# Optimization experiments

Hardware: AMD Instinct MI355X
Metric: run time of the kernel (lower is better)

Reference implementation:

```python
import jax, jax.numpy as jnp
import numpy as np
from jax import lax

DN = ('NCH', 'OIH', 'NCH')

def conv1d(x, w, b, pad=0):
    y = lax.conv_general_dilated(x, w, window_strides=(1,), padding=[(pad, pad)], dimension_numbers=DN)
    return y + b[None, :, None]

def conv_transpose1d(x, w_torch, b):
    # torch ConvTranspose1d weight: [C_in, C_out, K]; equivalent to full conv with flipped kernel
    k = w_torch.shape[-1]
    w = jnp.flip(jnp.transpose(w_torch, (1, 0, 2)), axis=-1)  # [C_out, C_in, K]
    y = lax.conv_general_dilated(x, w, window_strides=(1,), padding=[(k - 1, k - 1)], dimension_numbers=DN)
    return y + b[None, :, None]

def converter(signal, w1, b1, w2, b2, wt, bt, w3, b3):
    h = jax.nn.relu(conv1d(signal, w1, b1))          # [B,10,n-2]
    h = jax.nn.relu(conv1d(h, w2, b2))               # [B,10,n-2]
    h = jax.nn.relu(conv_transpose1d(h, wt, bt))     # [B,10,n]
    h = jax.nn.sigmoid(conv1d(h, w3, b3))            # [B,2,n]
    return h

def setup_inputs() -> dict:
    key = jax.random.key(0)
    ks = jax.random.split(key, 12)
    B, C, n = 32, 128, 8192
    signal = jax.random.normal(ks[0], (B, C, n), dtype=jnp.float32)
    curr_diag = jax.random.uniform(ks[1], (B, n - 1), dtype=jnp.float32) + 0.5
    s = 0.1
    return {
        'signal': signal,
        'curr_diag': curr_diag,
        'index_diag': 1,
        'w1': jax.random.normal(ks[2], (10, C, 3), dtype=jnp.float32) * s,
        'b1': jax.random.normal(ks[3], (10,), dtype=jnp.float32) * s,
        'w2': jax.random.normal(ks[4], (10, 10, 1), dtype=jnp.float32) * s,
        'b2': jax.random.normal(ks[5], (10,), dtype=jnp.float32) * s,
        'wt': jax.random.normal(ks[6], (10, 10, 3), dtype=jnp.float32) * s,
        'bt': jax.random.normal(ks[7], (10,), dtype=jnp.float32) * s,
        'w3': jax.random.normal(ks[8], (2, 10, 1), dtype=jnp.float32) * s,
        'b3': jax.random.normal(ks[9], (2,), dtype=jnp.float32) * s,
        'const': jnp.float32(0.99),
    }

def reference(signal, curr_diag, index_diag, w1, b1, w2, b2, wt, bt, w3, b3, const):
    n = signal.shape[-1]
    lr = converter(signal, w1, b1, w2, b2, wt, bt, w3, b3)  # [B,2,n]
    left, right = lr[:, 0, :], lr[:, 1, :]
    # diag_len = n - index_diag; next diag has length diag_len - 1
    mass_in = curr_diag[:, 1:] * right[:, 1:n - index_diag]
    mass_in = mass_in + curr_diag[:, :-1] * left[:, index_diag:n - 1]
    mass_out = right[:, 0:n - index_diag - 1] + left[:, index_diag + 1:n]
    next_diag = const * mass_in / mass_out
    next_diag = jnp.log(next_diag)
    next_diag = next_diag - jnp.mean(next_diag)
    return next_diag
```

## Files before the change

### kernel.cpp

```cpp
#include <hip/hip_runtime.h>
#include <math.h>

#define B     32
#define CIN   128
#define NN    8192
#define N1    8190
#define N1P   8192
#define CH    10
#define CHUNK 16
#define ROWF  260
#define ROWF2 268

__global__ void k0_prep(const float* __restrict__ w1, float* __restrict__ wT)
{
    const int i = blockIdx.x * 256 + threadIdx.x;
    if (i < CIN * 32) {
        const int ci = i >> 5, r = i & 31;
        float v = 0.f;
        if (r < 30) {
            const int o = r / 3, k = r - o * 3;
            v = w1[(o * CIN + ci) * 3 + k];
        }
        wT[i] = v;
    }
}

__global__ __launch_bounds__(256, 4) void k1_conv12(
    const float* __restrict__ sig, const float* __restrict__ wT, const float* __restrict__ b1,
    const float* __restrict__ w2, const float* __restrict__ b2, float* __restrict__ h2out)
{
    __shared__ float ls[CHUNK * ROWF];
    const int tid = threadIdx.x;
    const int b   = blockIdx.y;
    const int t0  = blockIdx.x * 256;
    const float* sb = sig + (size_t)b * CIN * NN;

    float4 pf[5];

    auto fetch = [&](int c) {
#pragma unroll
        for (int k = 0; k < 5; ++k) {
            const int li = tid + k * 256;
            if (k == 4 && tid >= 16) break;
            const int row = li / 65, col = li - row * 65;
            const int g = t0 + col * 4;
            const float* p = sb + (size_t)(c * CHUNK + row) * NN + g;
            float4 v = {0.f, 0.f, 0.f, 0.f};
            if (g + 3 < NN) v = *(const float4*)p;
            else {
                if (g + 0 < NN) v.x = p[0];
                if (g + 1 < NN) v.y = p[1];
                if (g + 2 < NN) v.z = p[2];
            }
            pf[k] = v;
        }
    };
    auto store_lds = [&]() {
#pragma unroll
        for (int k = 0; k < 5; ++k) {
            const int li = tid + k * 256;
            if (k == 4 && tid >= 16) break;
            const int row = li / 65, col = li - row * 65;
            *(float4*)&ls[row * ROWF + col * 4] = pf[k];
        }
    };

    float y[CH];
#pragma unroll
    for (int o = 0; o < CH; ++o) y[o] = b1[o];

    fetch(0);
    for (int c = 0; c < CIN / CHUNK; ++c) {
        __syncthreads();
        store_lds();
        __syncthreads();
        if (c < CIN / CHUNK - 1) fetch(c + 1);

        const float* wbase = wT + c * CHUNK * 32;
#pragma unroll
        for (int cl = 0; cl < CHUNK; ++cl) {
            const float s0 = ls[cl * ROWF + tid + 0];
            const float s1 = ls[cl * ROWF + tid + 1];
            const float s2 = ls[cl * ROWF + tid + 2];
            const float* wrow = wbase + cl * 32;
#pragma unroll
            for (int o = 0; o < CH; ++o) {
                y[o] = fmaf(wrow[o * 3 + 0], s0, y[o]);
                y[o] = fmaf(wrow[o * 3 + 1], s1, y[o]);
                y[o] = fmaf(wrow[o * 3 + 2], s2, y[o]);
            }
        }
    }

    const int t = t0 + tid;
    if (t < N1) {
#pragma unroll
        for (int o = 0; o < CH; ++o) y[o] = fmaxf(y[o], 0.f);
#pragma unroll
        for (int o = 0; o < CH; ++o) {
            float a = b2[o];
#pragma unroll
            for (int i = 0; i < CH; ++i) a = fmaf(w2[o * CH + i], y[i], a);
            h2out[((size_t)b * CH + o) * N1P + t] = fmaxf(a, 0.f);
        }
    }
}

__global__ __launch_bounds__(256, 4) void k2_fused(
    const float* __restrict__ h2, const float* __restrict__ cd,
    const float* __restrict__ wt, const float* __restrict__ bt,
    const float* __restrict__ w3, const float* __restrict__ b3,
    const float* __restrict__ cstp, float* __restrict__ outv, float* __restrict__ bsums)
{
    __shared__ float hs[CH * ROWF2];
    __shared__ float lsh[260], rsh[260];
    __shared__ float red[256];
    const int tid = threadIdx.x;
    const int b   = blockIdx.y;
    const int t0  = blockIdx.x * 256;
    const float* hb = h2 + (size_t)b * CH * N1P;

    for (int li = tid; li < 660; li += 256) {
        const int row = li / 66, col = li - row * 66;
        const int g = t0 - 4 + col * 4;
        const float* p = hb + (size_t)row * N1P + g;
        float4 v = {0.f, 0.f, 0.f, 0.f};
        if (g >= 0 && g + 3 < N1) v = *(const float4*)p;
        else {
            if (g + 0 >= 0 && g + 0 < N1) v.x = p[0];
            if (g + 1 >= 0 && g + 1 < N1) v.y = p[1];
            if (g + 2 >= 0 && g + 2 < N1) v.z = p[2];
            if (g + 3 >= 0 && g + 3 < N1) v.w = p[3];
        }
        *(float4*)&hs[row * ROWF2 + col * 4] = v;
    }
    __syncthreads();

    auto computeLR = [&](int sidx) {
        float acc[CH];
#pragma unroll
        for (int o = 0; o < CH; ++o) acc[o] = bt[o];
#pragma unroll
        for (int i = 0; i < CH; ++i) {
            const float a2 = hs[i * ROWF2 + sidx + 2];
            const float a3 = hs[i * ROWF2 + sidx + 3];
            const float a4 = hs[i * ROWF2 + sidx + 4];
            const float* wp = wt + i * CH * 3;
#pragma unroll
            for (int o = 0; o < CH; ++o) {
                acc[o] = fmaf(wp[o * 3 + 0], a4, acc[o]);
                acc[o] = fmaf(wp[o * 3 + 1], a3, acc[o]);
                acc[o] = fmaf(wp[o * 3 + 2], a2, acc[o]);
            }
        }
        float l = b3[0], r = b3[1];
#pragma unroll
        for (int o = 0; o < CH; ++o) {
            const float h3 = fmaxf(acc[o], 0.f);
            l = fmaf(w3[o],      h3, l);
            r = fmaf(w3[CH + o], h3, r);
        }
        lsh[sidx] = 1.f / (1.f + __expf(-l));
        rsh[sidx] = 1.f / (1.f + __expf(-r));
    };

    computeLR(tid);
    if (tid < 3) computeLR(256 + tid);
    __syncthreads();

    const int t = t0 + tid;
    float v = 0.f;
    if (t < N1) {
        const float c0 = cd[(size_t)b * (NN - 1) + t];
        const float c1 = cd[(size_t)b * (NN - 1) + t + 1];
        const float mi = c1 * rsh[tid + 1] + c0 * lsh[tid + 1];
        const float mo = rsh[tid] + lsh[tid + 2];
        v = __logf(cstp[0] * mi / mo);
        outv[(size_t)b * N1 + t] = v;
    }

    red[tid] = v;
    __syncthreads();
#pragma unroll
    for (int s = 128; s > 0; s >>= 1) {
        if (tid < s) red[tid] += red[tid + s];
        __syncthreads();
    }
    if (tid == 0) bsums[blockIdx.y * gridDim.x + blockIdx.x] = red[0];
}

__global__ __launch_bounds__(256) void k3_mean(const float* __restrict__ bsums, float* __restrict__ meanp)
{
    __shared__ float red[256];
    float s = 0.f;
    for (int i = threadIdx.x; i < 1024; i += 256) s += bsums[i];
    red[threadIdx.x] = s;
    __syncthreads();
#pragma unroll
    for (int st = 128; st > 0; st >>= 1) {
        if (threadIdx.x < st) red[threadIdx.x] += red[threadIdx.x + st];
        __syncthreads();
    }
    if (threadIdx.x == 0) meanp[0] = red[0] / (float)(B * N1);
}

__global__ __launch_bounds__(256) void k4_sub(float* __restrict__ outv, const float* __restrict__ meanp, int n)
{
    const int i = blockIdx.x * 256 + threadIdx.x;
    if (i < n) outv[i] -= meanp[0];
}

extern "C" void kernel_launch(void* const* d_in, const int* in_sizes, int n_in,
                              void* d_out, int out_size, void* d_ws, size_t ws_size,
                              hipStream_t stream)
{
    const float* sig = (const float*)d_in[0];
    const float* cd  = (const float*)d_in[1];
    const float* w1  = (const float*)d_in[3];
    const float* b1  = (const float*)d_in[4];
    const float* w2  = (const float*)d_in[5];
    const float* b2  = (const float*)d_in[6];
    const float* wt  = (const float*)d_in[7];
    const float* bt  = (const float*)d_in[8];
    const float* w3  = (const float*)d_in[9];
    const float* b3  = (const float*)d_in[10];
    const float* cst = (const float*)d_in[11];

    float* outv = (float*)d_out;

    float* ws   = (float*)d_ws;
    float* wT   = ws;
    float* h2   = wT + CIN * 32;
    float* bsum = h2 + (size_t)B * CH * N1P;
    float* mean = bsum + 1024;

    dim3 blk(256);
    dim3 g1(32, B);

    k0_prep  <<<dim3(16), blk, 0, stream>>>(w1, wT);
    k1_conv12<<<g1, blk, 0, stream>>>(sig, wT, b1, w2, b2, h2);
    k2_fused <<<g1, blk, 0, stream>>>(h2, cd, wt, bt, w3, b3, cst, outv, bsum);
    k3_mean  <<<dim3(1), blk, 0, stream>>>(bsum, mean);
    k4_sub   <<<dim3((out_size + 255) / 256), blk, 0, stream>>>(outv, mean, out_size);
}
```

Baseline: 255.2 us.

## Replace LDS staging with direct global loads and fuse mean-subtract kernels

The first conv kernel drops the LDS tile and barriers. Each thread now loads its three shifted inputs straight from global memory, using a register double-buffer across 8-channel groups and relying on the cache for the overlapping neighbour loads. The second kernel likewise reads h2 from global instead of staging it in shared memory. The separate mean and subtract kernels are merged so that every block redundantly reduces the 1024 partial sums and then subtracts, which removes a launch. The trade-off is roughly three times as many global load instructions, plus register pressure now that launch_bounds no longer requests a minimum block count.

After: 265.1 us. 3.9% more time.

```diff
diff --git a/kernel.cpp b/kernel.cpp
--- a/kernel.cpp
+++ b/kernel.cpp
@@ -1,15 +1,12 @@
 #include <hip/hip_runtime.h>
 #include <math.h>
 
-#define B     32
-#define CIN   128
-#define NN    8192
-#define N1    8190
-#define N1P   8192
-#define CH    10
-#define CHUNK 16
-#define ROWF  260
-#define ROWF2 268
+#define B    32
+#define CIN  128
+#define NN   8192
+#define N1   8190
+#define N1P  8192
+#define CH   10
 
 __global__ void k0_prep(const float* __restrict__ w1, float* __restrict__ wT)
 {
@@ -25,74 +22,52 @@
     }
 }
 
-__global__ __launch_bounds__(256, 4) void k1_conv12(
+__global__ __launch_bounds__(256) void k1_conv12(
     const float* __restrict__ sig, const float* __restrict__ wT, const float* __restrict__ b1,
     const float* __restrict__ w2, const float* __restrict__ b2, float* __restrict__ h2out)
 {
-    __shared__ float ls[CHUNK * ROWF];
     const int tid = threadIdx.x;
     const int b   = blockIdx.y;
-    const int t0  = blockIdx.x * 256;
-    const float* sb = sig + (size_t)b * CIN * NN;
-
-    float4 pf[5];
-
-    auto fetch = [&](int c) {
-#pragma unroll
-        for (int k = 0; k < 5; ++k) {
-            const int li = tid + k * 256;
-            if (k == 4 && tid >= 16) break;
-            const int row = li / 65, col = li - row * 65;
-            const int g = t0 + col * 4;
-            const float* p = sb + (size_t)(c * CHUNK + row) * NN + g;
-            float4 v = {0.f, 0.f, 0.f, 0.f};
-            if (g + 3 < NN) v = *(const float4*)p;
-            else {
-                if (g + 0 < NN) v.x = p[0];
-                if (g + 1 < NN) v.y = p[1];
-                if (g + 2 < NN) v.z = p[2];
+    const int t   = blockIdx.x * 256 + tid;
+    const int tc  = (t < N1 - 1) ? t : (N1 - 1);
+    const float* sp = sig + (size_t)b * CIN * NN + tc;
+
+    float y[CH];
+#pragma unroll
+    for (int o = 0; o < CH; ++o) y[o] = b1[o];
+
+    float ax[8], ay[8], az[8];
+    float bx[8], by[8], bz[8];
+
+    auto load = [&](float* x0, float* x1, float* x2, int c) {
+#pragma unroll
+        for (int j = 0; j < 8; ++j) {
+            const float* p = sp + (size_t)(c * 8 + j) * NN;
+            x0[j] = p[0]; x1[j] = p[1]; x2[j] = p[2];
+        }
+    };
+    auto comp = [&](const float* x0, const float* x1, const float* x2, int c) {
+        const float* wbase = wT + c * 8 * 32;
+#pragma unroll
+        for (int j = 0; j < 8; ++j) {
+            const float* wrow = wbase + j * 32;
+#pragma unroll
+            for (int o = 0; o < CH; ++o) {
+                y[o] = fmaf(wrow[o * 3 + 0], x0[j], y[o]);
+                y[o] = fmaf(wrow[o * 3 + 1], x1[j], y[o]);
+                y[o] = fmaf(wrow[o * 3 + 2], x2[j], y[o]);
             }
-            pf[k] = v;
         }
     };
-    auto store_lds = [&]() {
-#pragma unroll
-        for (int k = 0; k < 5; ++k) {
-            const int li = tid + k * 256;
-            if (k == 4 && tid >= 16) break;
-            const int row = li / 65, col = li - row * 65;
-            *(float4*)&ls[row * ROWF + col * 4] = pf[k];
-        }
-    };
-
-    float y[CH];
-#pragma unroll
-    for (int o = 0; o < CH; ++o) y[o] = b1[o];
-
-    fetch(0);
-    for (int c = 0; c < CIN / CHUNK; ++c) {
-        __syncthreads();
-        store_lds();
-        __syncthreads();
-        if (c < CIN / CHUNK - 1) fetch(c + 1);
-
-        const float* wbase = wT + c * CHUNK * 32;
-#pragma unroll
-        for (int cl = 0; cl < CHUNK; ++cl) {
-            const float s0 = ls[cl * ROWF + tid + 0];
-            const float s1 = ls[cl * ROWF + tid + 1];
-            const float s2 = ls[cl * ROWF + tid + 2];
-            const float* wrow = wbase + cl * 32;
-#pragma unroll
-            for (int o = 0; o < CH; ++o) {
-                y[o] = fmaf(wrow[o * 3 + 0], s0, y[o]);
-                y[o] = fmaf(wrow[o * 3 + 1], s1, y[o]);
-                y[o] = fmaf(wrow[o * 3 + 2], s2, y[o]);
-            }
-        }
-    }
-
-    const int t = t0 + tid;
+
+    load(ax, ay, az, 0);
+    for (int c = 0; c < 16; c += 2) {
+        load(bx, by, bz, c + 1);
+        comp(ax, ay, az, c);
+        if (c + 2 < 16) load(ax, ay, az, c + 2);
+        comp(bx, by, bz, c + 1);
+    }
+
     if (t < N1) {
 #pragma unroll
         for (int o = 0; o < CH; ++o) y[o] = fmaxf(y[o], 0.f);
@@ -106,13 +81,12 @@
     }
 }
 
-__global__ __launch_bounds__(256, 4) void k2_fused(
+__global__ __launch_bounds__(256) void k2_fused(
     const float* __restrict__ h2, const float* __restrict__ cd,
     const float* __restrict__ wt, const float* __restrict__ bt,
     const float* __restrict__ w3, const float* __restrict__ b3,
     const float* __restrict__ cstp, float* __restrict__ outv, float* __restrict__ bsums)
 {
-    __shared__ float hs[CH * ROWF2];
     __shared__ float lsh[260], rsh[260];
     __shared__ float red[256];
     const int tid = threadIdx.x;
@@ -120,37 +94,23 @@
     const int t0  = blockIdx.x * 256;
     const float* hb = h2 + (size_t)b * CH * N1P;
 
-    for (int li = tid; li < 660; li += 256) {
-        const int row = li / 66, col = li - row * 66;
-        const int g = t0 - 4 + col * 4;
-        const float* p = hb + (size_t)row * N1P + g;
-        float4 v = {0.f, 0.f, 0.f, 0.f};
-        if (g >= 0 && g + 3 < N1) v = *(const float4*)p;
-        else {
-            if (g + 0 >= 0 && g + 0 < N1) v.x = p[0];
-            if (g + 1 >= 0 && g + 1 < N1) v.y = p[1];
-            if (g + 2 >= 0 && g + 2 < N1) v.z = p[2];
-            if (g + 3 >= 0 && g + 3 < N1) v.w = p[3];
-        }
-        *(float4*)&hs[row * ROWF2 + col * 4] = v;
-    }
-    __syncthreads();
-
     auto computeLR = [&](int sidx) {
+        const int s = t0 + sidx;
         float acc[CH];
 #pragma unroll
         for (int o = 0; o < CH; ++o) acc[o] = bt[o];
 #pragma unroll
         for (int i = 0; i < CH; ++i) {
-            const float a2 = hs[i * ROWF2 + sidx + 2];
-            const float a3 = hs[i * ROWF2 + sidx + 3];
-            const float a4 = hs[i * ROWF2 + sidx + 4];
+            const float* hp = hb + (size_t)i * N1P;
+            const float v0 = (s < N1)            ? hp[s]     : 0.f;
+            const float v1 = (s >= 1 && s <= N1) ? hp[s - 1] : 0.f;
+            const float v2 = (s >= 2)            ? hp[s - 2] : 0.f;
             const float* wp = wt + i * CH * 3;
 #pragma unroll
             for (int o = 0; o < CH; ++o) {
-                acc[o] = fmaf(wp[o * 3 + 0], a4, acc[o]);
-                acc[o] = fmaf(wp[o * 3 + 1], a3, acc[o]);
-                acc[o] = fmaf(wp[o * 3 + 2], a2, acc[o]);
+                acc[o] = fmaf(wp[o * 3 + 0], v0, acc[o]);
+                acc[o] = fmaf(wp[o * 3 + 1], v1, acc[o]);
+                acc[o] = fmaf(wp[o * 3 + 2], v2, acc[o]);
             }
         }
         float l = b3[0], r = b3[1];
@@ -165,7 +125,7 @@
     };
 
     computeLR(tid);
-    if (tid < 3) computeLR(256 + tid);
+    if (tid < 3 && t0 + 256 + tid < NN) computeLR(256 + tid);
     __syncthreads();
 
     const int t = t0 + tid;
@@ -189,25 +149,25 @@
     if (tid == 0) bsums[blockIdx.y * gridDim.x + blockIdx.x] = red[0];
 }
 
-__global__ __launch_bounds__(256) void k3_mean(const float* __restrict__ bsums, float* __restrict__ meanp)
+__global__ __launch_bounds__(256) void k3_meansub(
+    const float* __restrict__ bsums, float* __restrict__ outv, int n)
 {
     __shared__ float red[256];
+    const int tid = threadIdx.x;
     float s = 0.f;
-    for (int i = threadIdx.x; i < 1024; i += 256) s += bsums[i];
-    red[threadIdx.x] = s;
+#pragma unroll
+    for (int i = 0; i < 4; ++i) s += bsums[tid + i * 256];
+    red[tid] = s;
     __syncthreads();
 #pragma unroll
     for (int st = 128; st > 0; st >>= 1) {
-        if (threadIdx.x < st) red[threadIdx.x] += red[threadIdx.x + st];
+        if (tid < st) red[tid] += red[tid + st];
         __syncthreads();
     }
-    if (threadIdx.x == 0) meanp[0] = red[0] / (float)(B * N1);
-}
-
-__global__ __launch_bounds__(256) void k4_sub(float* __restrict__ outv, const float* __restrict__ meanp, int n)
-{
-    const int i = blockIdx.x * 256 + threadIdx.x;
-    if (i < n) outv[i] -= meanp[0];
+    const float mean = red[0] / (float)(B * N1);
+    __syncthreads();
+    const int i = blockIdx.x * 256 + tid;
+    if (i < n) outv[i] -= mean;
 }
 
 extern "C" void kernel_launch(void* const* d_in, const int* in_sizes, int n_in,
@@ -232,14 +192,12 @@
     float* wT   = ws;
     float* h2   = wT + CIN * 32;
     float* bsum = h2 + (size_t)B * CH * N1P;
-    float* mean = bsum + 1024;
 
     dim3 blk(256);
     dim3 g1(32, B);
 
-    k0_prep  <<<dim3(16), blk, 0, stream>>>(w1, wT);
-    k1_conv12<<<g1, blk, 0, stream>>>(sig, wT, b1, w2, b2, h2);
-    k2_fused <<<g1, blk, 0, stream>>>(h2, cd, wt, bt, w3, b3, cst, outv, bsum);
-    k3_mean  <<<dim3(1), blk, 0, stream>>>(bsum, mean);
-    k4_sub   <<<dim3((out_size + 255) / 256), blk, 0, stream>>>(outv, mean, out_size);
-}
+    k0_prep   <<<dim3(16), blk, 0, stream>>>(w1, wT);
+    k1_conv12 <<<g1, blk, 0, stream>>>(sig, wT, b1, w2, b2, h2);
+    k2_fused  <<<g1, blk, 0, stream>>>(h2, cd, wt, bt, w3, b3, cst, outv, bsum);
+    k3_meansub<<<dim3((out_size + 255) / 256), blk, 0, stream>>>(bsum, outv, out_size);
+}
```
